# Optimization experiments

Measured on AMD Instinct MI355X. Metric: run time of the kernel, lower is better.

## Reference

```python
import jax, jax.numpy as jnp
import numpy as np

SCALE = 10.0
TEMP = 0.5
SIM_TH = 0.7
EPOCH = 1
KL_WEIGHT = max(0.5 * (1 - EPOCH / 60), 0.1)
NEG_INF = -1e30


def _normalize(x, eps=1e-12):
    n = jnp.linalg.norm(x, axis=-1, keepdims=True)
    return x / jnp.maximum(n, eps)


def setup_inputs() -> dict:
    key = jax.random.key(0)
    ks = jax.random.split(key, 6)
    P, B, D, N, K = 4, 128, 512, 32768, 10
    # 0.02 scale keeps pairwise distances O(1) so exp(-SCALE*dist) does not underflow
    feature = jax.random.normal(ks[0], (P, B, D), jnp.float32) * 0.02
    text_feature = jax.random.normal(ks[1], (B, P, D), jnp.float32) * 0.02
    centers = jax.random.normal(ks[2], (P, N, D), jnp.float32) * 0.02
    position = jax.random.randint(ks[3], (B,), 0, N)
    cross_indices = jax.random.randint(ks[4], (B, K), 0, N)
    vid = jax.random.randint(ks[5], (N,), 0, 751)
    return {"feature": feature, "text_feature": text_feature, "centers": centers,
            "position": position, "cross_indices": cross_indices, "vid": vid}


def _align_loss(feature, text_feature):
    # feature: [P,B,D]; text_feature: [B,P,D] (detached in original)
    img = _normalize(feature)
    txt = _normalize(jax.lax.stop_gradient(jnp.transpose(text_feature, (1, 0, 2))))
    img_sim = jnp.einsum('pbd,pcd->pbc', img, img) / TEMP   # [P,B,B]
    txt_sim = jnp.einsum('pbd,pcd->pbc', txt, txt) / TEMP
    mask = (img_sim > SIM_TH) & (txt_sim > SIM_TH)
    valid = mask.any(-1)                                   # [P,B] row/col validity
    colm = valid[:, None, :]                               # mask over columns
    il = jnp.where(colm, img_sim, NEG_INF)
    tl = jnp.where(colm, txt_sim, NEG_INF)
    img_logp = jax.nn.log_softmax(il, -1)
    txt_logp = jax.nn.log_softmax(tl, -1)                  # fully detached (txt detached)
    txt_prob = jnp.exp(txt_logp)
    img_logp_sg = jax.lax.stop_gradient(img_logp)
    img_prob = jnp.exp(img_logp_sg)
    # F.kl_div(input=log q, target=p) = sum p*(log p - log q), batchmean over valid rows
    kl1 = jnp.sum(jnp.where(colm, txt_prob * (txt_logp - img_logp), 0.0), -1)      # [P,B]
    kl2 = jnp.sum(jnp.where(colm, img_prob * (img_logp_sg - txt_logp), 0.0), -1)
    nvalid = valid.sum(-1)                                 # [P]
    r1 = jnp.sum(jnp.where(valid, kl1, 0.0), -1)
    r2 = jnp.sum(jnp.where(valid, kl2, 0.0), -1)
    per_part = 0.5 * (r1 + r2) / jnp.maximum(nvalid, 1)
    return jnp.sum(jnp.where(nvalid > 0, per_part, 0.0))


def _contrastive_loss(feature, centers, position, cross_indices):
    P, B, D = feature.shape
    N = centers.shape[1]
    pos_feats = jnp.take(centers, cross_indices, axis=1)   # [P,B,K,D]
    fn2 = jnp.sum(feature * feature, -1)                   # [P,B]
    pn2 = jnp.sum(pos_feats * pos_feats, -1)               # [P,B,K]
    pd2 = fn2[..., None] + pn2 - 2.0 * jnp.einsum('pbd,pbkd->pbk', feature, pos_feats)
    pos_dist = jnp.sqrt(jnp.maximum(pd2, 1e-12))           # [P,B,K]
    cn2 = jnp.sum(centers * centers, -1)                   # [P,N]
    nd2 = fn2[..., None] + cn2[:, None, :] - 2.0 * jnp.einsum('pbd,pnd->pbn', feature, centers)
    neg_dist = jnp.sqrt(jnp.maximum(nd2, 1e-12))           # [P,B,N]
    neg_mask = (jnp.ones((N,), bool)
                .at[cross_indices.reshape(-1)].set(False)
                .at[position].set(False))
    x = jnp.log(jnp.sum(jnp.exp(-SCALE * pos_dist), -1))   # [P,B]
    ey = jnp.exp(-SCALE * neg_dist) * neg_mask[None, None, :].astype(neg_dist.dtype)
    y = jnp.log(jnp.sum(ey, -1))                           # [P,B]
    l = jnp.sum(y - x, -1) / B                             # per-part, div by feature.size(1)
    l = jnp.where(jnp.isnan(l), 0.0, l)
    return jnp.sum(l) / P


def reference(feature, text_feature, centers, position, cross_indices, vid):
    align_loss = _align_loss(feature, text_feature)
    contrastive_loss = _contrastive_loss(feature, centers, position, cross_indices)
    total_loss = contrastive_loss + KL_WEIGHT * align_loss
    pos_vid = jnp.take(vid, cross_indices, axis=0)         # [B,K]
    return total_loss, contrastive_loss, align_loss, pos_vid
```

## Files before the change

### kernel.cpp

```cpp
#include <hip/hip_runtime.h>
#include <hip/hip_bf16.h>
#include <math.h>

#define P_ 4
#define B_ 128
#define D_ 512
#define N_ 32768
#define K_ 10
#define TNB 128
#define NT2 (N_ / TNB)
#define BK2 32
#define NCH (D_ / BK2)
#define KP2 40

typedef __attribute__((ext_vector_type(8))) short bf16x8;
typedef __attribute__((ext_vector_type(4))) float f32x4;

static __device__ __forceinline__ float block_sum_128(float v, float* sh) {
    const int t = threadIdx.x;
    sh[t] = v; __syncthreads();
    #pragma unroll
    for (int s = 64; s > 0; s >>= 1) { if (t < s) sh[t] += sh[t + s]; __syncthreads(); }
    float r = sh[0]; __syncthreads();
    return r;
}

static __device__ __forceinline__ uint2 pack_bf16x4(float4 v) {
    union { __hip_bfloat162 h; unsigned u; } lo, hi;
    lo.h = __float22bfloat162_rn(make_float2(v.x, v.y));
    hi.h = __float22bfloat162_rn(make_float2(v.z, v.w));
    uint2 r; r.x = lo.u; r.y = hi.u;
    return r;
}

__global__ void mask_init_kernel(float* __restrict__ m) {
    int i = blockIdx.x * 256 + threadIdx.x;
    if (i < N_) m[i] = 1.0f;
}
__global__ void mask_zero_kernel(const int* __restrict__ cross,
                                 const int* __restrict__ pos,
                                 float* __restrict__ m) {
    int i = blockIdx.x * 256 + threadIdx.x;
    if (i < B_ * K_) m[cross[i]] = 0.0f;
    else if (i < B_ * K_ + B_) m[pos[i - B_ * K_]] = 0.0f;
}

__global__ void norm_kernel(const float* __restrict__ feature,
                            const float* __restrict__ text_feature,
                            float* __restrict__ img, float* __restrict__ txt,
                            float* __restrict__ fn2) {
    const int pb = blockIdx.x;
    const int p = pb >> 7, b = pb & 127;
    const int which = blockIdx.y;
    const int t = threadIdx.x;
    const float* src = (which == 0) ? feature + (size_t)pb * D_
                                    : text_feature + ((size_t)b * P_ + p) * D_;
    float v0 = src[t], v1 = src[t + 256];
    __shared__ float sred[256];
    sred[t] = v0 * v0 + v1 * v1;
    __syncthreads();
    #pragma unroll
    for (int s = 128; s > 0; s >>= 1) { if (t < s) sred[t] += sred[t + s]; __syncthreads(); }
    const float ss = sred[0];
    const float inv = 1.0f / fmaxf(sqrtf(ss), 1e-12f);
    float* dst = (which == 0) ? img : txt;
    dst[(size_t)pb * D_ + t] = v0 * inv;
    dst[(size_t)pb * D_ + t + 256] = v1 * inv;
    if (which == 0 && t == 0) fn2[pb] = ss;
}

__global__ void sim_kernel(const float* __restrict__ img,
                           const float* __restrict__ txt,
                           float* __restrict__ img_sim,
                           float* __restrict__ txt_sim,
                           float* __restrict__ validf) {
    const int p = blockIdx.x;
    const int b0 = blockIdx.y * 2;
    const int c = threadIdx.x;
    __shared__ float ai[2][D_];
    __shared__ float at[2][D_];
    __shared__ int flags[2];
    #pragma unroll
    for (int i = 0; i < 8; ++i) {
        int idx = c + i * 128;
        int row = idx >> 9, d = idx & 511;
        ai[row][d] = img[(size_t)(p * B_ + b0 + row) * D_ + d];
        at[row][d] = txt[(size_t)(p * B_ + b0 + row) * D_ + d];
    }
    if (c < 2) flags[c] = 0;
    __syncthreads();
    float di[2] = {0, 0};
    float dt[2] = {0, 0};
    const float* ic = img + (size_t)(p * B_ + c) * D_;
    const float* tc = txt + (size_t)(p * B_ + c) * D_;
    for (int d = 0; d < D_; d += 4) {
        float4 vi = *(const float4*)(ic + d);
        float4 vt = *(const float4*)(tc + d);
        #pragma unroll
        for (int i = 0; i < 2; ++i) {
            di[i] += ai[i][d] * vi.x + ai[i][d + 1] * vi.y + ai[i][d + 2] * vi.z + ai[i][d + 3] * vi.w;
            dt[i] += at[i][d] * vt.x + at[i][d + 1] * vt.y + at[i][d + 2] * vt.z + at[i][d + 3] * vt.w;
        }
    }
    #pragma unroll
    for (int i = 0; i < 2; ++i) {
        float is = 2.0f * di[i];
        float ts = 2.0f * dt[i];
        img_sim[(size_t)(p * B_ + b0 + i) * B_ + c] = is;
        txt_sim[(size_t)(p * B_ + b0 + i) * B_ + c] = ts;
        if (is > 0.7f && ts > 0.7f) flags[i] = 1;
    }
    __syncthreads();
    if (c < 2) validf[p * B_ + b0 + c] = (float)flags[c];
}

__global__ __launch_bounds__(256) void kl_kernel(
    const float* __restrict__ img_sim,
    const float* __restrict__ txt_sim,
    const float* __restrict__ validf,
    float* __restrict__ klrow) {
    const int l = threadIdx.x & 63;
    const int wv = threadIdx.x >> 6;
    const int p = blockIdx.x;
    const int r = blockIdx.y * 4 + wv;
    const size_t base = (size_t)(p * B_ + r) * B_;
    const bool v0 = validf[p * B_ + l] > 0.5f;
    const bool v1 = validf[p * B_ + 64 + l] > 0.5f;
    const float il0 = v0 ? img_sim[base + l] : -1e30f;
    const float il1 = v1 ? img_sim[base + 64 + l] : -1e30f;
    const float tl0 = v0 ? txt_sim[base + l] : -1e30f;
    const float tl1 = v1 ? txt_sim[base + 64 + l] : -1e30f;
    float mi = fmaxf(il0, il1), mt = fmaxf(tl0, tl1);
    #pragma unroll
    for (int off = 32; off > 0; off >>= 1) {
        mi = fmaxf(mi, __shfl_xor(mi, off));
        mt = fmaxf(mt, __shfl_xor(mt, off));
    }
    float si = expf(il0 - mi) + expf(il1 - mi);
    float st = expf(tl0 - mt) + expf(tl1 - mt);
    #pragma unroll
    for (int off = 32; off > 0; off >>= 1) {
        si += __shfl_xor(si, off);
        st += __shfl_xor(st, off);
    }
    const float lsei = mi + logf(si);
    const float lset = mt + logf(st);
    float term = 0.0f;
    if (v0) {
        float lpi = il0 - lsei, lpt = tl0 - lset;
        term += expf(lpt) * (lpt - lpi) + expf(lpi) * (lpi - lpt);
    }
    if (v1) {
        float lpi = il1 - lsei, lpt = tl1 - lset;
        term += expf(lpt) * (lpt - lpi) + expf(lpi) * (lpi - lpt);
    }
    #pragma unroll
    for (int off = 32; off > 0; off >>= 1) term += __shfl_xor(term, off);
    if (l == 0) klrow[p * B_ + r] = (validf[p * B_ + r] > 0.5f) ? term : 0.0f;
}

__global__ void posx_kernel(const float* __restrict__ feature,
                            const float* __restrict__ centers,
                            const float* __restrict__ fn2,
                            const int* __restrict__ cross,
                            float* __restrict__ xarr) {
    const int pb = blockIdx.x;
    const int p = pb >> 7, b = pb & 127;
    const int l = threadIdx.x;
    const float* f = feature + (size_t)pb * D_;
    float4 f0 = *(const float4*)(f + l * 4);
    float4 f1 = *(const float4*)(f + 256 + l * 4);
    const float fn2v = fn2[pb];
    float ex = 0.0f;
    #pragma unroll
    for (int k = 0; k < K_; ++k) {
        int idx = cross[b * K_ + k];
        const float* cp = centers + ((size_t)p * N_ + idx) * D_;
        float4 c0 = *(const float4*)(cp + l * 4);
        float4 c1 = *(const float4*)(cp + 256 + l * 4);
        float dot = f0.x * c0.x + f0.y * c0.y + f0.z * c0.z + f0.w * c0.w
                  + f1.x * c1.x + f1.y * c1.y + f1.z * c1.z + f1.w * c1.w;
        float pn2 = c0.x * c0.x + c0.y * c0.y + c0.z * c0.z + c0.w * c0.w
                  + c1.x * c1.x + c1.y * c1.y + c1.z * c1.z + c1.w * c1.w;
        #pragma unroll
        for (int off = 32; off > 0; off >>= 1) {
            dot += __shfl_down(dot, off);
            pn2 += __shfl_down(pn2, off);
        }
        if (l == 0) {
            float d2 = fn2v + pn2 - 2.0f * dot;
            ex += expf(-10.0f * sqrtf(fmaxf(d2, 1e-12f)));
        }
    }
    if (l == 0) xarr[pb] = logf(ex);
}

__global__ __launch_bounds__(256) void neg_mfma_kernel(
    const float* __restrict__ feature,
    const float* __restrict__ centers,
    const float* __restrict__ fn2,
    const float* __restrict__ maskf,
    float* __restrict__ Spart) {
    const int tile = blockIdx.x;
    const int p = blockIdx.y;
    const int n0g = tile * TNB;
    const int t = threadIdx.x;
    const int l = t & 63;
    const int w = t >> 6;
    const int m0w = (w & 1) * 64;
    const int n0w = (w >> 1) * 64;

    __shared__ unsigned short As[2][128 * KP2];
    __shared__ unsigned short Bs[2][128 * KP2];
    __shared__ float cn2s[128];
    __shared__ float red[128];
    __shared__ float fn2s[128];

    if (t < 128) { red[t] = 0.0f; fn2s[t] = fn2[p * B_ + t]; }

    f32x4 acc[4][4];
    #pragma unroll
    for (int i = 0; i < 4; ++i)
        #pragma unroll
        for (int j = 0; j < 4; ++j) acc[i][j] = (f32x4)0.0f;

    float c2acc[4] = {0.0f, 0.0f, 0.0f, 0.0f};

    const float* Ab = feature + (size_t)p * B_ * D_;
    const float* Bb = centers + ((size_t)p * N_ + n0g) * D_;

    const int f8 = t & 7;
    const int r0 = t >> 3;

    float4 va[4], vb[4];
    #pragma unroll
    for (int i = 0; i < 4; ++i) {
        const int row = r0 + 32 * i;
        va[i] = *(const float4*)(Ab + (size_t)row * D_ + f8 * 4);
        vb[i] = *(const float4*)(Bb + (size_t)row * D_ + f8 * 4);
    }
    #pragma unroll
    for (int i = 0; i < 4; ++i) {
        const int row = r0 + 32 * i;
        *(uint2*)&As[0][row * KP2 + f8 * 4] = pack_bf16x4(va[i]);
        *(uint2*)&Bs[0][row * KP2 + f8 * 4] = pack_bf16x4(vb[i]);
        c2acc[i] += vb[i].x * vb[i].x + vb[i].y * vb[i].y
                  + vb[i].z * vb[i].z + vb[i].w * vb[i].w;
    }
    __syncthreads();

    const int ko = (l >> 4) * 8;
    for (int c = 0; c < NCH; ++c) {
        const int cur = c & 1, nxt = cur ^ 1;
        const int kk = (c + 1) * BK2;
        if (c < NCH - 1) {
            #pragma unroll
            for (int i = 0; i < 4; ++i) {
                const int row = r0 + 32 * i;
                va[i] = *(const float4*)(Ab + (size_t)row * D_ + kk + f8 * 4);
                vb[i] = *(const float4*)(Bb + (size_t)row * D_ + kk + f8 * 4);
            }
        }
        bf16x8 af[4], bfr[4];
        #pragma unroll
        for (int i = 0; i < 4; ++i) {
            af[i]  = *(const bf16x8*)&As[cur][(m0w + i * 16 + (l & 15)) * KP2 + ko];
            bfr[i] = *(const bf16x8*)&Bs[cur][(n0w + i * 16 + (l & 15)) * KP2 + ko];
        }
        #pragma unroll
        for (int i = 0; i < 4; ++i)
            #pragma unroll
            for (int j = 0; j < 4; ++j)
                acc[i][j] = __builtin_amdgcn_mfma_f32_16x16x32_bf16(
                    af[i], bfr[j], acc[i][j], 0, 0, 0);
        if (c < NCH - 1) {
            #pragma unroll
            for (int i = 0; i < 4; ++i) {
                const int row = r0 + 32 * i;
                *(uint2*)&As[nxt][row * KP2 + f8 * 4] = pack_bf16x4(va[i]);
                *(uint2*)&Bs[nxt][row * KP2 + f8 * 4] = pack_bf16x4(vb[i]);
                c2acc[i] += vb[i].x * vb[i].x + vb[i].y * vb[i].y
                          + vb[i].z * vb[i].z + vb[i].w * vb[i].w;
            }
        }
        __syncthreads();
    }

    #pragma unroll
    for (int i = 0; i < 4; ++i) {
        float s = c2acc[i];
        s += __shfl_xor(s, 1); s += __shfl_xor(s, 2); s += __shfl_xor(s, 4);
        if (f8 == 0) cn2s[r0 + 32 * i] = s;
    }
    __syncthreads();

    float c2l[4], mkl[4];
    #pragma unroll
    for (int j = 0; j < 4; ++j) {
        const int col = n0w + j * 16 + (l & 15);
        c2l[j] = cn2s[col];
        mkl[j] = maskf[n0g + col];
    }
    #pragma unroll
    for (int i = 0; i < 4; ++i) {
        #pragma unroll
        for (int r = 0; r < 4; ++r) {
            const int row = m0w + i * 16 + (l >> 4) * 4 + r;
            const float fv = fn2s[row];
            float s = 0.0f;
            #pragma unroll
            for (int j = 0; j < 4; ++j) {
                const float nd2 = fv + c2l[j] - 2.0f * acc[i][j][r];
                s += mkl[j] * __expf(-10.0f * sqrtf(fmaxf(nd2, 1e-12f)));
            }
            s += __shfl_xor(s, 1); s += __shfl_xor(s, 2);
            s += __shfl_xor(s, 4); s += __shfl_xor(s, 8);
            if ((l & 15) == 0) atomicAdd(&red[row], s);
        }
    }
    __syncthreads();
    if (t < 128) Spart[(size_t)(p * B_ + t) * NT2 + tile] = red[t];
}

__global__ void red_kernel(const float* __restrict__ Spart,
                           const float* __restrict__ xarr,
                           float* __restrict__ diff) {
    const int pb = blockIdx.x;
    const int t = threadIdx.x;
    __shared__ float sh[128];
    const float* sp = Spart + (size_t)pb * NT2;
    float s = sp[t] + sp[t + 128];
    float S = block_sum_128(s, sh);
    if (t == 0) diff[pb] = logf(S) - xarr[pb];
}

__global__ void final_kernel(const float* __restrict__ validf,
                             const float* __restrict__ klrow,
                             const float* __restrict__ diff,
                             const int* __restrict__ cross,
                             const int* __restrict__ vid,
                             float* __restrict__ out) {
    const int t = threadIdx.x;
    __shared__ float sh[128];
    __shared__ float accum[2];
    if (t == 0) { accum[0] = 0.0f; accum[1] = 0.0f; }
    __syncthreads();
    for (int p = 0; p < P_; ++p) {
        float nv = block_sum_128(validf[p * B_ + t], sh);
        float ks = block_sum_128(klrow[p * B_ + t], sh);
        float ds = block_sum_128(diff[p * B_ + t], sh);
        if (t == 0) {
            float lp = ds / (float)B_;
            if (!(lp != lp)) accum[0] += lp;
            if (nv > 0.5f) accum[1] += 0.5f * ks / fmaxf(nv, 1.0f);
        }
        __syncthreads();
    }
    if (t == 0) {
        float contrastive = accum[0] / (float)P_;
        float align = accum[1];
        out[1] = contrastive;
        out[2] = align;
        out[0] = contrastive + 0.49166666666666664f * align;
    }
    #pragma unroll
    for (int k = 0; k < K_; ++k) {
        const int i = k * 128 + t;
        out[3 + i] = (float)vid[cross[i]];
    }
}

extern "C" void kernel_launch(void* const* d_in, const int* in_sizes, int n_in,
                              void* d_out, int out_size, void* d_ws, size_t ws_size,
                              hipStream_t stream) {
    const float* feature      = (const float*)d_in[0];
    const float* text_feature = (const float*)d_in[1];
    const float* centers      = (const float*)d_in[2];
    const int*   position     = (const int*)d_in[3];
    const int*   cross        = (const int*)d_in[4];
    const int*   vid          = (const int*)d_in[5];
    float* out = (float*)d_out;

    float* ws      = (float*)d_ws;
    float* img     = ws;
    float* txt     = img + (size_t)P_ * B_ * D_;
    float* fn2     = txt + (size_t)P_ * B_ * D_;
    float* img_sim = fn2 + P_ * B_;
    float* txt_sim = img_sim + P_ * B_ * B_;
    float* validf  = txt_sim + P_ * B_ * B_;
    float* klrow   = validf + P_ * B_;
    float* xarr    = klrow + P_ * B_;
    float* maskf   = xarr + P_ * B_;
    float* diff    = maskf + N_;
    float* Spart   = diff + P_ * B_;

    mask_init_kernel<<<N_ / 256, 256, 0, stream>>>(maskf);
    mask_zero_kernel<<<(B_ * K_ + B_ + 255) / 256, 256, 0, stream>>>(cross, position, maskf);
    norm_kernel<<<dim3(P_ * B_, 2), 256, 0, stream>>>(feature, text_feature, img, txt, fn2);
    sim_kernel<<<dim3(P_, B_ / 2), 128, 0, stream>>>(img, txt, img_sim, txt_sim, validf);
    kl_kernel<<<dim3(P_, B_ / 4), 256, 0, stream>>>(img_sim, txt_sim, validf, klrow);
    posx_kernel<<<P_ * B_, 64, 0, stream>>>(feature, centers, fn2, cross, xarr);
    neg_mfma_kernel<<<dim3(NT2, P_), 256, 0, stream>>>(feature, centers, fn2, maskf, Spart);
    red_kernel<<<P_ * B_, 128, 0, stream>>>(Spart, xarr, diff);
    final_kernel<<<1, 128, 0, stream>>>(validf, klrow, diff, cross, vid, out);
}
```

Measured before the change: 444.9 us.

## Fuse normalization, mask and reduction kernels; deepen prefetch in MFMA negative-distance kernel

Removes the mask init/zero, norm and red kernels. Norms are now computed inside sim, posx and the MFMA kernel, the mask is built per tile in LDS, and per-tile sums are atomically accumulated into a global Ssum that final_kernel consumes. The MFMA kernel now prefetches two chunks ahead in registers, uses a lighter LDS barrier and sets launch bounds for two blocks per CU. This cuts launch count and global round-trips, at the cost of float atomics (nondeterministic summation order) and higher register pressure.

```diff
diff --git a/kernel.cpp b/kernel.cpp
--- a/kernel.cpp
+++ b/kernel.cpp
@@ -16,6 +16,8 @@
 typedef __attribute__((ext_vector_type(8))) short bf16x8;
 typedef __attribute__((ext_vector_type(4))) float f32x4;
 
+#define LDS_BARRIER() asm volatile("s_waitcnt lgkmcnt(0)\n\ts_barrier" ::: "memory")
+
 static __device__ __forceinline__ float block_sum_128(float v, float* sh) {
     const int t = threadIdx.x;
     sh[t] = v; __syncthreads();
@@ -33,79 +35,56 @@
     return r;
 }
 
-__global__ void mask_init_kernel(float* __restrict__ m) {
-    int i = blockIdx.x * 256 + threadIdx.x;
-    if (i < N_) m[i] = 1.0f;
-}
-__global__ void mask_zero_kernel(const int* __restrict__ cross,
-                                 const int* __restrict__ pos,
-                                 float* __restrict__ m) {
-    int i = blockIdx.x * 256 + threadIdx.x;
-    if (i < B_ * K_) m[cross[i]] = 0.0f;
-    else if (i < B_ * K_ + B_) m[pos[i - B_ * K_]] = 0.0f;
-}
-
-__global__ void norm_kernel(const float* __restrict__ feature,
-                            const float* __restrict__ text_feature,
-                            float* __restrict__ img, float* __restrict__ txt,
-                            float* __restrict__ fn2) {
-    const int pb = blockIdx.x;
-    const int p = pb >> 7, b = pb & 127;
-    const int which = blockIdx.y;
-    const int t = threadIdx.x;
-    const float* src = (which == 0) ? feature + (size_t)pb * D_
-                                    : text_feature + ((size_t)b * P_ + p) * D_;
-    float v0 = src[t], v1 = src[t + 256];
-    __shared__ float sred[256];
-    sred[t] = v0 * v0 + v1 * v1;
-    __syncthreads();
-    #pragma unroll
-    for (int s = 128; s > 0; s >>= 1) { if (t < s) sred[t] += sred[t + s]; __syncthreads(); }
-    const float ss = sred[0];
-    const float inv = 1.0f / fmaxf(sqrtf(ss), 1e-12f);
-    float* dst = (which == 0) ? img : txt;
-    dst[(size_t)pb * D_ + t] = v0 * inv;
-    dst[(size_t)pb * D_ + t + 256] = v1 * inv;
-    if (which == 0 && t == 0) fn2[pb] = ss;
-}
-
-__global__ void sim_kernel(const float* __restrict__ img,
-                           const float* __restrict__ txt,
-                           float* __restrict__ img_sim,
-                           float* __restrict__ txt_sim,
-                           float* __restrict__ validf) {
+__global__ __launch_bounds__(128) void sim_kernel(
+    const float* __restrict__ feature,
+    const float* __restrict__ text_feature,
+    float* __restrict__ img_sim,
+    float* __restrict__ txt_sim,
+    float* __restrict__ validf,
+    float* __restrict__ Ssum) {
     const int p = blockIdx.x;
     const int b0 = blockIdx.y * 2;
     const int c = threadIdx.x;
+    if (blockIdx.y == 0) Ssum[p * B_ + c] = 0.0f;
     __shared__ float ai[2][D_];
     __shared__ float at[2][D_];
+    __shared__ float cinv_i[128];
+    __shared__ float cinv_t[128];
     __shared__ int flags[2];
     #pragma unroll
     for (int i = 0; i < 8; ++i) {
         int idx = c + i * 128;
         int row = idx >> 9, d = idx & 511;
-        ai[row][d] = img[(size_t)(p * B_ + b0 + row) * D_ + d];
-        at[row][d] = txt[(size_t)(p * B_ + b0 + row) * D_ + d];
+        ai[row][d] = feature[(size_t)(p * B_ + b0 + row) * D_ + d];
+        at[row][d] = text_feature[((size_t)(b0 + row) * P_ + p) * D_ + d];
     }
     if (c < 2) flags[c] = 0;
     __syncthreads();
     float di[2] = {0, 0};
     float dt[2] = {0, 0};
-    const float* ic = img + (size_t)(p * B_ + c) * D_;
-    const float* tc = txt + (size_t)(p * B_ + c) * D_;
+    float ssi = 0.0f, sst = 0.0f;
+    const float* fc = feature + (size_t)(p * B_ + c) * D_;
+    const float* tc = text_feature + ((size_t)c * P_ + p) * D_;
     for (int d = 0; d < D_; d += 4) {
-        float4 vi = *(const float4*)(ic + d);
+        float4 vi = *(const float4*)(fc + d);
         float4 vt = *(const float4*)(tc + d);
+        ssi += vi.x * vi.x + vi.y * vi.y + vi.z * vi.z + vi.w * vi.w;
+        sst += vt.x * vt.x + vt.y * vt.y + vt.z * vt.z + vt.w * vt.w;
         #pragma unroll
         for (int i = 0; i < 2; ++i) {
-            di[i] += ai[i][d] * vi.x + ai[i][d + 1] * vi.y + ai[i][d + 2] * vi.z + ai[i][d + 3] * vi.w;
-            dt[i] += at[i][d] * vt.x + at[i][d + 1] * vt.y + at[i][d + 2] * vt.z + at[i][d + 3] * vt.w;
-        }
-    }
+            float4 a4 = *(const float4*)&ai[i][d];
+            float4 t4 = *(const float4*)&at[i][d];
+            di[i] += a4.x * vi.x + a4.y * vi.y + a4.z * vi.z + a4.w * vi.w;
+            dt[i] += t4.x * vt.x + t4.y * vt.y + t4.z * vt.z + t4.w * vt.w;
+        }
+    }
+    cinv_i[c] = 1.0f / fmaxf(sqrtf(ssi), 1e-12f);
+    cinv_t[c] = 1.0f / fmaxf(sqrtf(sst), 1e-12f);
+    __syncthreads();
     #pragma unroll
     for (int i = 0; i < 2; ++i) {
-        float is = 2.0f * di[i];
-        float ts = 2.0f * dt[i];
+        float is = 2.0f * di[i] * cinv_i[b0 + i] * cinv_i[c];
+        float ts = 2.0f * dt[i] * cinv_t[b0 + i] * cinv_t[c];
         img_sim[(size_t)(p * B_ + b0 + i) * B_ + c] = is;
         txt_sim[(size_t)(p * B_ + b0 + i) * B_ + c] = ts;
         if (is > 0.7f && ts > 0.7f) flags[i] = 1;
@@ -161,7 +140,6 @@
 
 __global__ void posx_kernel(const float* __restrict__ feature,
                             const float* __restrict__ centers,
-                            const float* __restrict__ fn2,
                             const int* __restrict__ cross,
                             float* __restrict__ xarr) {
     const int pb = blockIdx.x;
@@ -170,7 +148,10 @@
     const float* f = feature + (size_t)pb * D_;
     float4 f0 = *(const float4*)(f + l * 4);
     float4 f1 = *(const float4*)(f + 256 + l * 4);
-    const float fn2v = fn2[pb];
+    float fs = f0.x * f0.x + f0.y * f0.y + f0.z * f0.z + f0.w * f0.w
+             + f1.x * f1.x + f1.y * f1.y + f1.z * f1.z + f1.w * f1.w;
+    #pragma unroll
+    for (int off = 32; off > 0; off >>= 1) fs += __shfl_down(fs, off);
     float ex = 0.0f;
     #pragma unroll
     for (int k = 0; k < K_; ++k) {
@@ -188,19 +169,19 @@
             pn2 += __shfl_down(pn2, off);
         }
         if (l == 0) {
-            float d2 = fn2v + pn2 - 2.0f * dot;
+            float d2 = fs + pn2 - 2.0f * dot;
             ex += expf(-10.0f * sqrtf(fmaxf(d2, 1e-12f)));
         }
     }
     if (l == 0) xarr[pb] = logf(ex);
 }
 
-__global__ __launch_bounds__(256) void neg_mfma_kernel(
+__global__ __launch_bounds__(256, 2) void neg_mfma_kernel(
     const float* __restrict__ feature,
     const float* __restrict__ centers,
-    const float* __restrict__ fn2,
-    const float* __restrict__ maskf,
-    float* __restrict__ Spart) {
+    const int* __restrict__ cross,
+    const int* __restrict__ position,
+    float* __restrict__ Ssum) {
     const int tile = blockIdx.x;
     const int p = blockIdx.y;
     const int n0g = tile * TNB;
@@ -213,10 +194,11 @@
     __shared__ unsigned short As[2][128 * KP2];
     __shared__ unsigned short Bs[2][128 * KP2];
     __shared__ float cn2s[128];
+    __shared__ float fn2s[128];
     __shared__ float red[128];
-    __shared__ float fn2s[128];
-
-    if (t < 128) { red[t] = 0.0f; fn2s[t] = fn2[p * B_ + t]; }
+    __shared__ float msk[128];
+
+    if (t < 128) { red[t] = 0.0f; msk[t] = 1.0f; }
 
     f32x4 acc[4][4];
     #pragma unroll
@@ -225,6 +207,7 @@
         for (int j = 0; j < 4; ++j) acc[i][j] = (f32x4)0.0f;
 
     float c2acc[4] = {0.0f, 0.0f, 0.0f, 0.0f};
+    float a2acc[4] = {0.0f, 0.0f, 0.0f, 0.0f};
 
     const float* Ab = feature + (size_t)p * B_ * D_;
     const float* Bb = centers + ((size_t)p * N_ + n0g) * D_;
@@ -232,40 +215,53 @@
     const int f8 = t & 7;
     const int r0 = t >> 3;
 
-    float4 va[4], vb[4];
-    #pragma unroll
-    for (int i = 0; i < 4; ++i) {
-        const int row = r0 + 32 * i;
-        va[i] = *(const float4*)(Ab + (size_t)row * D_ + f8 * 4);
-        vb[i] = *(const float4*)(Bb + (size_t)row * D_ + f8 * 4);
-    }
-    #pragma unroll
-    for (int i = 0; i < 4; ++i) {
-        const int row = r0 + 32 * i;
-        *(uint2*)&As[0][row * KP2 + f8 * 4] = pack_bf16x4(va[i]);
-        *(uint2*)&Bs[0][row * KP2 + f8 * 4] = pack_bf16x4(vb[i]);
-        c2acc[i] += vb[i].x * vb[i].x + vb[i].y * vb[i].y
-                  + vb[i].z * vb[i].z + vb[i].w * vb[i].w;
-    }
-    __syncthreads();
+    float4 va0[4], vb0[4], va1[4], vb1[4];
+
+#define LOAD_SET(va, vb, kk) \
+    _Pragma("unroll") \
+    for (int i = 0; i < 4; ++i) { \
+        const int row = r0 + 32 * i; \
+        va[i] = *(const float4*)(Ab + (size_t)row * D_ + (kk) + f8 * 4); \
+        vb[i] = *(const float4*)(Bb + (size_t)row * D_ + (kk) + f8 * 4); \
+    }
+
+#define PACK_SET(va, vb, buf) \
+    _Pragma("unroll") \
+    for (int i = 0; i < 4; ++i) { \
+        const int row = r0 + 32 * i; \
+        *(uint2*)&As[buf][row * KP2 + f8 * 4] = pack_bf16x4(va[i]); \
+        *(uint2*)&Bs[buf][row * KP2 + f8 * 4] = pack_bf16x4(vb[i]); \
+        a2acc[i] += va[i].x * va[i].x + va[i].y * va[i].y \
+                  + va[i].z * va[i].z + va[i].w * va[i].w; \
+        c2acc[i] += vb[i].x * vb[i].x + vb[i].y * vb[i].y \
+                  + vb[i].z * vb[i].z + vb[i].w * vb[i].w; \
+    }
+
+    LOAD_SET(va0, vb0, 0)
+    LOAD_SET(va1, vb1, BK2)
+    PACK_SET(va0, vb0, 0)
+    LDS_BARRIER();
+
+    for (int i = t; i < B_ * K_ + B_; i += 256) {
+        const int v = (i < B_ * K_) ? cross[i] : position[i - B_ * K_];
+        const unsigned rr = (unsigned)(v - n0g);
+        if (rr < (unsigned)TNB) msk[rr] = 0.0f;
+    }
 
     const int ko = (l >> 4) * 8;
+    const int fr = l & 15;
+    #pragma unroll
     for (int c = 0; c < NCH; ++c) {
-        const int cur = c & 1, nxt = cur ^ 1;
-        const int kk = (c + 1) * BK2;
-        if (c < NCH - 1) {
-            #pragma unroll
-            for (int i = 0; i < 4; ++i) {
-                const int row = r0 + 32 * i;
-                va[i] = *(const float4*)(Ab + (size_t)row * D_ + kk + f8 * 4);
-                vb[i] = *(const float4*)(Bb + (size_t)row * D_ + kk + f8 * 4);
-            }
+        const int cur = c & 1;
+        if (c + 2 < NCH) {
+            if (cur == 0) { LOAD_SET(va0, vb0, (c + 2) * BK2) }
+            else          { LOAD_SET(va1, vb1, (c + 2) * BK2) }
         }
         bf16x8 af[4], bfr[4];
         #pragma unroll
         for (int i = 0; i < 4; ++i) {
-            af[i]  = *(const bf16x8*)&As[cur][(m0w + i * 16 + (l & 15)) * KP2 + ko];
-            bfr[i] = *(const bf16x8*)&Bs[cur][(n0w + i * 16 + (l & 15)) * KP2 + ko];
+            af[i]  = *(const bf16x8*)&As[cur][(m0w + i * 16 + fr) * KP2 + ko];
+            bfr[i] = *(const bf16x8*)&Bs[cur][(n0w + i * 16 + fr) * KP2 + ko];
         }
         #pragma unroll
         for (int i = 0; i < 4; ++i)
@@ -273,33 +269,32 @@
             for (int j = 0; j < 4; ++j)
                 acc[i][j] = __builtin_amdgcn_mfma_f32_16x16x32_bf16(
                     af[i], bfr[j], acc[i][j], 0, 0, 0);
-        if (c < NCH - 1) {
-            #pragma unroll
-            for (int i = 0; i < 4; ++i) {
-                const int row = r0 + 32 * i;
-                *(uint2*)&As[nxt][row * KP2 + f8 * 4] = pack_bf16x4(va[i]);
-                *(uint2*)&Bs[nxt][row * KP2 + f8 * 4] = pack_bf16x4(vb[i]);
-                c2acc[i] += vb[i].x * vb[i].x + vb[i].y * vb[i].y
-                          + vb[i].z * vb[i].z + vb[i].w * vb[i].w;
-            }
-        }
-        __syncthreads();
-    }
+        if (c + 1 < NCH) {
+            if (cur == 0) { PACK_SET(va1, vb1, 1) }
+            else          { PACK_SET(va0, vb0, 0) }
+        }
+        LDS_BARRIER();
+    }
+
+#undef LOAD_SET
+#undef PACK_SET
 
     #pragma unroll
     for (int i = 0; i < 4; ++i) {
         float s = c2acc[i];
         s += __shfl_xor(s, 1); s += __shfl_xor(s, 2); s += __shfl_xor(s, 4);
-        if (f8 == 0) cn2s[r0 + 32 * i] = s;
-    }
-    __syncthreads();
+        float sa = a2acc[i];
+        sa += __shfl_xor(sa, 1); sa += __shfl_xor(sa, 2); sa += __shfl_xor(sa, 4);
+        if (f8 == 0) { cn2s[r0 + 32 * i] = s; fn2s[r0 + 32 * i] = sa; }
+    }
+    LDS_BARRIER();
 
     float c2l[4], mkl[4];
     #pragma unroll
     for (int j = 0; j < 4; ++j) {
-        const int col = n0w + j * 16 + (l & 15);
+        const int col = n0w + j * 16 + fr;
         c2l[j] = cn2s[col];
-        mkl[j] = maskf[n0g + col];
+        mkl[j] = msk[col];
     }
     #pragma unroll
     for (int i = 0; i < 4; ++i) {
@@ -315,28 +310,17 @@
             }
             s += __shfl_xor(s, 1); s += __shfl_xor(s, 2);
             s += __shfl_xor(s, 4); s += __shfl_xor(s, 8);
-            if ((l & 15) == 0) atomicAdd(&red[row], s);
-        }
-    }
-    __syncthreads();
-    if (t < 128) Spart[(size_t)(p * B_ + t) * NT2 + tile] = red[t];
-}
-
-__global__ void red_kernel(const float* __restrict__ Spart,
-                           const float* __restrict__ xarr,
-                           float* __restrict__ diff) {
-    const int pb = blockIdx.x;
-    const int t = threadIdx.x;
-    __shared__ float sh[128];
-    const float* sp = Spart + (size_t)pb * NT2;
-    float s = sp[t] + sp[t + 128];
-    float S = block_sum_128(s, sh);
-    if (t == 0) diff[pb] = logf(S) - xarr[pb];
+            if (fr == 0) atomicAdd(&red[row], s);
+        }
+    }
+    LDS_BARRIER();
+    if (t < 128) atomicAdd(&Ssum[p * B_ + t], red[t]);
 }
 
 __global__ void final_kernel(const float* __restrict__ validf,
                              const float* __restrict__ klrow,
-                             const float* __restrict__ diff,
+                             const float* __restrict__ xarr,
+                             const float* __restrict__ Ssum,
                              const int* __restrict__ cross,
                              const int* __restrict__ vid,
                              float* __restrict__ out) {
@@ -348,7 +332,8 @@
     for (int p = 0; p < P_; ++p) {
         float nv = block_sum_128(validf[p * B_ + t], sh);
         float ks = block_sum_128(klrow[p * B_ + t], sh);
-        float ds = block_sum_128(diff[p * B_ + t], sh);
+        float dv = logf(Ssum[p * B_ + t]) - xarr[p * B_ + t];
+        float ds = block_sum_128(dv, sh);
         if (t == 0) {
             float lp = ds / (float)B_;
             if (!(lp != lp)) accum[0] += lp;
@@ -382,25 +367,18 @@
     float* out = (float*)d_out;
 
     float* ws      = (float*)d_ws;
-    float* img     = ws;
-    float* txt     = img + (size_t)P_ * B_ * D_;
-    float* fn2     = txt + (size_t)P_ * B_ * D_;
-    float* img_sim = fn2 + P_ * B_;
-    float* txt_sim = img_sim + P_ * B_ * B_;
-    float* validf  = txt_sim + P_ * B_ * B_;
+    float* img_sim = ws;
+    float* txt_sim = img_sim + (size_t)P_ * B_ * B_;
+    float* validf  = txt_sim + (size_t)P_ * B_ * B_;
     float* klrow   = validf + P_ * B_;
     float* xarr    = klrow + P_ * B_;
-    float* maskf   = xarr + P_ * B_;
-    float* diff    = maskf + N_;
-    float* Spart   = diff + P_ * B_;
-
-    mask_init_kernel<<<N_ / 256, 256, 0, stream>>>(maskf);
-    mask_zero_kernel<<<(B_ * K_ + B_ + 255) / 256, 256, 0, stream>>>(cross, position, maskf);
-    norm_kernel<<<dim3(P_ * B_, 2), 256, 0, stream>>>(feature, text_feature, img, txt, fn2);
-    sim_kernel<<<dim3(P_, B_ / 2), 128, 0, stream>>>(img, txt, img_sim, txt_sim, validf);
+    float* Ssum    = xarr + P_ * B_;
+
+    sim_kernel<<<dim3(P_, B_ / 2), 128, 0, stream>>>(feature, text_feature,
+                                                     img_sim, txt_sim, validf, Ssum);
     kl_kernel<<<dim3(P_, B_ / 4), 256, 0, stream>>>(img_sim, txt_sim, validf, klrow);
-    posx_kernel<<<P_ * B_, 64, 0, stream>>>(feature, centers, fn2, cross, xarr);
-    neg_mfma_kernel<<<dim3(NT2, P_), 256, 0, stream>>>(feature, centers, fn2, maskf, Spart);
-    red_kernel<<<P_ * B_, 128, 0, stream>>>(Spart, xarr, diff);
-    final_kernel<<<1, 128, 0, stream>>>(validf, klrow, diff, cross, vid, out);
-}
+    posx_kernel<<<P_ * B_, 64, 0, stream>>>(feature, centers, cross, xarr);
+    neg_mfma_kernel<<<dim3(NT2, P_), 256, 0, stream>>>(feature, centers, cross,
+                                                       position, Ssum);
+    final_kernel<<<1, 128, 0, stream>>>(validf, klrow, xarr, Ssum, cross, vid, out);
+}
```

After: 584.6 us. 31.4% more time.
